# Performance work log

Measured on AMD Instinct MI355X. Metric: run time of the kernel, lower is better.

Reference implementation:

```python
import jax, jax.numpy as jnp
import numpy as np

N_NODES = 100000
N_EDGES = 1600000
N_ETYPES = 3
IN_FEATS = 128
HEADS = 4
OUT_FEATS = 16
EDGE_FEATS = 64
NEG_SLOPE = 0.2


def setup_inputs() -> dict:
    key = jax.random.key(0)
    ks = jax.random.split(key, 10)
    return {
        "x": jax.random.normal(ks[0], (N_NODES, IN_FEATS), jnp.float32),
        "W": jax.random.normal(ks[1], (IN_FEATS, HEADS * OUT_FEATS), jnp.float32) * 0.05,
        "W_e": jax.random.normal(ks[2], (EDGE_FEATS, HEADS * EDGE_FEATS), jnp.float32) * 0.05,
        "attn_l": jax.random.normal(ks[3], (HEADS, OUT_FEATS), jnp.float32) * 0.1,
        "attn_r": jax.random.normal(ks[4], (HEADS, OUT_FEATS), jnp.float32) * 0.1,
        "attn_e": jax.random.normal(ks[5], (HEADS, EDGE_FEATS), jnp.float32) * 0.1,
        "edge_emb": jax.random.normal(ks[6], (N_ETYPES, EDGE_FEATS), jnp.float32),
        "src": jax.random.randint(ks[7], (N_EDGES,), 0, N_NODES, jnp.int32),
        "dst": jax.random.randint(ks[8], (N_EDGES,), 0, N_NODES, jnp.int32),
        "etype": jax.random.randint(ks[9], (N_EDGES,), 0, N_ETYPES, jnp.int32),
    }


def reference(x, W, W_e, attn_l, attn_r, attn_e, edge_emb, src, dst, etype):
    N = x.shape[0]
    H, D = attn_l.shape
    # node projection: [N, H, D]
    feat = (x @ W).reshape(N, H, D)
    # per-node attention halves: [N, H]
    el = jnp.einsum("nhd,hd->nh", feat, attn_l)
    er = jnp.einsum("nhd,hd->nh", feat, attn_r)
    # per-etype edge term: [T, H]
    e_feat = (edge_emb @ W_e).reshape(edge_emb.shape[0], H, -1)
    ee = jnp.einsum("the,he->th", e_feat, attn_e)
    # per-edge pre-softmax score: [E, H]
    s = el[src] + er[dst] + ee[etype]
    s = jnp.where(s > 0, s, NEG_SLOPE * s)  # leaky_relu
    # edge softmax over incoming edges of each dst node (homogeneous graph)
    m = jax.ops.segment_max(s, dst, num_segments=N)
    e = jnp.exp(s - m[dst])
    z = jax.ops.segment_sum(e, dst, num_segments=N)
    a = e / z[dst]  # [E, H]
    # u_mul_e + sum aggregation: [N, H, D]
    msg = feat[src] * a[:, :, None]
    rst = jax.ops.segment_sum(msg, dst, num_segments=N)
    return rst, a
```

## Files before the change

### kernel.cpp

```cpp
#include <hip/hip_runtime.h>
#include <hip/hip_bf16.h>

#define N_NODES   100000
#define N_EDGES   1600000
#define N_ETYPES  3
#define IN_FEATS  128
#define HEADS     4
#define OUT_FEATS 16
#define EDGE_FEATS 64
#define HD        64
#define NEG_SLOPE 0.2f
#define MAXD_LDS  128

#define NBUCK     800
#define NPB       125
#define PBLK      400
#define EPB       4000
#define BCAP      2560
#define FROWS     32


typedef short s16x8 __attribute__((ext_vector_type(8)));
typedef float f32x4 __attribute__((ext_vector_type(4)));

__device__ __forceinline__ short f2bs(float f) {
    __hip_bfloat16 h = __float2bfloat16(f);
    return *reinterpret_cast<short*>(&h);
}

__global__ __launch_bounds__(256) void wt_prep_kernel(
    const float* __restrict__ W, short* __restrict__ WTb)
{
    const int t = blockIdx.x * 256 + threadIdx.x;
    const int k = t >> 6, n = t & 63;
    WTb[n * IN_FEATS + k] = f2bs(W[t]);
}

#define XS_STRIDE 136
__global__ __launch_bounds__(256) void feat_el_er_kernel(
    const float* __restrict__ x,
    const short* __restrict__ WTb,
    const float* __restrict__ attn_l,
    const float* __restrict__ attn_r,
    const float* __restrict__ edge_emb,
    const float* __restrict__ W_e,
    const float* __restrict__ attn_e,
    __hip_bfloat16* __restrict__ featb,
    float* __restrict__ el,
    float* __restrict__ eriz,
    float* __restrict__ ee,
    int* __restrict__ cnt)
{
    const int t = threadIdx.x;

    if (blockIdx.x == N_NODES / FROWS) {
        for (int j = t; j < NBUCK; j += 256) cnt[j] = 0;
        const int wv = t >> 6, e = t & 63;
        for (int j = wv; j < N_ETYPES * HEADS; j += 4) {
            const int ty = j >> 2, h = j & 3;
            float ef = 0.f;
#pragma unroll
            for (int k = 0; k < EDGE_FEATS; ++k)
                ef += edge_emb[ty * EDGE_FEATS + k] *
                      W_e[k * (HEADS * EDGE_FEATS) + h * EDGE_FEATS + e];
            float v = ef * attn_e[h * EDGE_FEATS + e];
#pragma unroll
            for (int m = 1; m < 64; m <<= 1) v += __shfl_xor(v, m, 64);
            if (e == 0) ee[ty * HEADS + h] = v;
        }
        return;
    }

    __shared__ short Xs[FROWS * XS_STRIDE];

    const int row0 = blockIdx.x * FROWS;
    {
        const int r = t >> 3, k0 = (t & 7) * 16;
        const float4* xg = (const float4*)(x + (size_t)(row0 + r) * IN_FEATS + k0);
        const float4 v0 = xg[0], v1 = xg[1], v2 = xg[2], v3 = xg[3];
        s16x8 p0, p1;
        p0[0] = f2bs(v0.x); p0[1] = f2bs(v0.y); p0[2] = f2bs(v0.z); p0[3] = f2bs(v0.w);
        p0[4] = f2bs(v1.x); p0[5] = f2bs(v1.y); p0[6] = f2bs(v1.z); p0[7] = f2bs(v1.w);
        p1[0] = f2bs(v2.x); p1[1] = f2bs(v2.y); p1[2] = f2bs(v2.z); p1[3] = f2bs(v2.w);
        p1[4] = f2bs(v3.x); p1[5] = f2bs(v3.y); p1[6] = f2bs(v3.z); p1[7] = f2bs(v3.w);
        *(s16x8*)&Xs[r * XS_STRIDE + k0]     = p0;
        *(s16x8*)&Xs[r * XS_STRIDE + k0 + 8] = p1;
    }

    const int w    = t >> 6;
    const int lane = t & 63;
    const int m    = lane & 15;
    const int q    = lane >> 4;

    s16x8 bfr[4];
#pragma unroll
    for (int kb = 0; kb < 4; ++kb)
        bfr[kb] = *(const s16x8*)(WTb + (size_t)(w * 16 + m) * IN_FEATS + kb * 32 + q * 8);

    const float al = attn_l[w * OUT_FEATS + m];
    const float ar = attn_r[w * OUT_FEATS + m];

    __syncthreads();

#pragma unroll
    for (int rg = 0; rg < 2; ++rg) {
        f32x4 acc = {0.f, 0.f, 0.f, 0.f};
#pragma unroll
        for (int kb = 0; kb < 4; ++kb) {
            const s16x8 af = *(const s16x8*)&Xs[(rg * 16 + m) * XS_STRIDE + kb * 32 + q * 8];
            acc = __builtin_amdgcn_mfma_f32_16x16x32_bf16(af, bfr[kb], acc, 0, 0, 0);
        }
#pragma unroll
        for (int r = 0; r < 4; ++r) {
            const int row = row0 + rg * 16 + q * 4 + r;
            featb[(size_t)row * HD + w * 16 + m] = __float2bfloat16(acc[r]);
            float cl = acc[r] * al;
            float cr = acc[r] * ar;
#pragma unroll
            for (int msk = 1; msk < 16; msk <<= 1) {
                cl += __shfl_xor(cl, msk, 64);
                cr += __shfl_xor(cr, msk, 64);
            }
            if (m == 0) {
                el[row * HEADS + w] = cl;
                eriz[(size_t)row * 8 + w] = cr;
            }
        }
    }
}

__global__ __launch_bounds__(256) void scatter_kernel(
    const int* __restrict__ src, const int* __restrict__ dst,
    const int* __restrict__ etype,
    int* __restrict__ cnt, int* __restrict__ sc_bucket)
{
    __shared__ int h[NBUCK];
    int buld[16];
    const int t = threadIdx.x, b = blockIdx.x;
    for (int j = t; j < NBUCK; j += 256) h[j] = 0;
    __syncthreads();
    const int e0 = b * EPB;
    int k = 0;
    for (int i = t; i < EPB; i += 256, ++k) {
        const int dn = dst[e0 + i];
        const int bu = dn / NPB;
        const int ld = dn - bu * NPB;
        buld[k] = bu | (ld << 16);
        atomicAdd(&h[bu], 1);
    }
    __syncthreads();
    for (int j = t; j < NBUCK; j += 256) {
        const int c = h[j];
        h[j] = j * BCAP + (c ? atomicAdd(&cnt[j], c) : 0);
    }
    __syncthreads();
    k = 0;
    for (int i = t; i < EPB; i += 256, ++k) {
        const int e  = e0 + i;
        const int bu = buld[k] & 0xFFFF;
        const int ld = buld[k] >> 16;
        const int slot = atomicAdd(&h[bu], 1);
        sc_bucket[slot] = src[e] | (etype[e] << 17) | (ld << 19);
    }
}

__global__ __launch_bounds__(256) void bucket_csr_kernel(
    const int* __restrict__ sc_bucket, const int* __restrict__ cnt,
    int* __restrict__ ptr, int* __restrict__ sc_csr)
{
    __shared__ int sbuf[BCAP];
    __shared__ int sdeg4[4][128];
    __shared__ int sdg[128];
    __shared__ int scur[128];
    __shared__ int red[4];
    const int t = threadIdx.x, b = blockIdx.x;
    const int wid = t >> 6;

    int acc = 0;
    for (int j = t; j < b; j += 256) acc += cnt[j];
#pragma unroll
    for (int m = 1; m < 64; m <<= 1) acc += __shfl_xor(acc, m, 64);
    if ((t & 63) == 0) red[wid] = acc;
    sdeg4[0][t & 127] = 0; sdeg4[1][t & 127] = 0;
    if (t < 128) { sdeg4[2][t] = 0; sdeg4[3][t] = 0; }
    __syncthreads();
    const int lo    = red[0] + red[1] + red[2] + red[3];
    const int count = cnt[b];
    const int base  = b * BCAP;
    const bool staged = (count <= BCAP);

    if (staged) {
        for (int i = t; i < count; i += 256) {
            const int v = sc_bucket[base + i];
            sbuf[i] = v;
            atomicAdd(&sdeg4[wid][(v >> 19) & 0x7F], 1);
        }
    } else {
        for (int i = t; i < count; i += 256)
            atomicAdd(&sdeg4[wid][(sc_bucket[base + i] >> 19) & 0x7F], 1);
    }
    __syncthreads();
    int orig = 0;
    if (t < 128) {
        orig = sdeg4[0][t] + sdeg4[1][t] + sdeg4[2][t] + sdeg4[3][t];
        sdg[t] = orig;
    }
    __syncthreads();
    for (int off = 1; off < 128; off <<= 1) {
        const int v = (t < 128 && t >= off) ? sdg[t - off] : 0;
        __syncthreads();
        if (t < 128) sdg[t] += v;
        __syncthreads();
    }
    if (t < 128) {
        const int excl = sdg[t] - orig;
        if (t < NPB) ptr[b * NPB + t] = lo + excl;
        scur[t] = lo + excl;
    }
    if (b == 0 && t == 0) ptr[N_NODES] = N_EDGES;
    __syncthreads();
    if (staged) {
        for (int i = t; i < count; i += 256) {
            const int v = sbuf[i];
            const int ld = (v >> 19) & 0x7F;
            const int slot = atomicAdd(&scur[ld], 1);
            sc_csr[slot] = v & 0x7FFFF;
        }
    } else {
        for (int i = t; i < count; i += 256) {
            const int v = sc_bucket[base + i];
            const int ld = (v >> 19) & 0x7F;
            const int slot = atomicAdd(&scur[ld], 1);
            sc_csr[slot] = v & 0x7FFFF;
        }
    }
}

__global__ __launch_bounds__(256) void agg_kernel(
    const int* __restrict__ sc_csr, const int* __restrict__ ptr,
    const float* __restrict__ el, float* __restrict__ eriz,
    const float* __restrict__ ee, const __hip_bfloat16* __restrict__ featb,
    float* __restrict__ rst)
{
    __shared__ float w_lds[4][MAXD_LDS * HEADS];
    __shared__ int   s_lds[4][MAXD_LDS];
    const int wid  = threadIdx.x >> 6;
    const int lane = threadIdx.x & 63;
    const int n    = blockIdx.x * 4 + wid;

    const int p0  = ptr[n];
    const int deg = ptr[n + 1] - p0;
    float* wl = w_lds[wid];
    int*   sl = s_lds[wid];
    const ushort* fb = (const ushort*)featb;

    if (deg <= MAXD_LDS) {
        const int eo = lane >> 2;
        const int hA = lane & 3;
        const float er_n = eriz[(size_t)n * 8 + hA];
        const float g0 = ee[hA], g1 = ee[HEADS + hA], g2 = ee[2 * HEADS + hA];

        float zacc = 0.f;
        for (int i0 = 0; i0 < deg; i0 += 32) {
            const int idxA = i0 + eo;
            const int idxB = i0 + 16 + eo;
            const bool pA = idxA < deg;
            const bool pB = idxB < deg;
            int vA = 0, vB = 0;
            if (pA) vA = sc_csr[p0 + idxA];
            if (pB) vB = sc_csr[p0 + idxB];
            float eA = 0.f, eB = 0.f;
            if (pA) eA = el[(vA & 0x1FFFF) * HEADS + hA];
            if (pB) eB = el[(vB & 0x1FFFF) * HEADS + hA];
            if (pA) {
                const int ty = vA >> 17;
                float s = eA + er_n + ((ty == 0) ? g0 : ((ty == 1) ? g1 : g2));
                s = s > 0.f ? s : NEG_SLOPE * s;
                const float w = __expf(s);
                wl[idxA * HEADS + hA] = w;
                if (hA == 0) sl[idxA] = vA & 0x1FFFF;
                zacc += w;
            }
            if (pB) {
                const int ty = vB >> 17;
                float s = eB + er_n + ((ty == 0) ? g0 : ((ty == 1) ? g1 : g2));
                s = s > 0.f ? s : NEG_SLOPE * s;
                const float w = __expf(s);
                wl[idxB * HEADS + hA] = w;
                if (hA == 0) sl[idxB] = vB & 0x1FFFF;
                zacc += w;
            }
        }
        zacc += __shfl_xor(zacc, 4, 64);
        zacc += __shfl_xor(zacc, 8, 64);
        zacc += __shfl_xor(zacc, 16, 64);
        zacc += __shfl_xor(zacc, 32, 64);
        if (lane < 4)
            eriz[(size_t)n * 8 + 4 + lane] = (deg > 0) ? __frcp_rn(zacc) : 0.f;

        const int q8 = lane >> 3;
        const int c8 = lane & 7;
        const int h8 = c8 >> 1;
        const float inv_z = (deg > 0) ? __frcp_rn(__shfl(zacc, h8, 64)) : 0.f;

        float a0 = 0.f, a1 = 0.f, a2 = 0.f, a3 = 0.f;
        float a4 = 0.f, a5 = 0.f, a6 = 0.f, a7 = 0.f;
        int i = 0;
        for (; i + 16 <= deg; i += 16) {
            const int idxA = i + q8, idxB = i + 8 + q8;
            const int sA = sl[idxA], sB = sl[idxB];
            const float wA = wl[idxA * HEADS + h8];
            const float wB = wl[idxB * HEADS + h8];
            const uint4 fA = *(const uint4*)(fb + ((size_t)sA << 6) + (c8 << 3));
            const uint4 fB = *(const uint4*)(fb + ((size_t)sB << 6) + (c8 << 3));
            a0 += __uint_as_float(fA.x << 16) * wA;
            a1 += __uint_as_float(fA.x & 0xFFFF0000u) * wA;
            a2 += __uint_as_float(fA.y << 16) * wA;
            a3 += __uint_as_float(fA.y & 0xFFFF0000u) * wA;
            a4 += __uint_as_float(fA.z << 16) * wA;
            a5 += __uint_as_float(fA.z & 0xFFFF0000u) * wA;
            a6 += __uint_as_float(fA.w << 16) * wA;
            a7 += __uint_as_float(fA.w & 0xFFFF0000u) * wA;
            a0 += __uint_as_float(fB.x << 16) * wB;
            a1 += __uint_as_float(fB.x & 0xFFFF0000u) * wB;
            a2 += __uint_as_float(fB.y << 16) * wB;
            a3 += __uint_as_float(fB.y & 0xFFFF0000u) * wB;
            a4 += __uint_as_float(fB.z << 16) * wB;
            a5 += __uint_as_float(fB.z & 0xFFFF0000u) * wB;
            a6 += __uint_as_float(fB.w << 16) * wB;
            a7 += __uint_as_float(fB.w & 0xFFFF0000u) * wB;
        }
        if (i + 8 <= deg) {
            const int idx = i + q8;
            const int sA = sl[idx];
            const float wA = wl[idx * HEADS + h8];
            const uint4 fA = *(const uint4*)(fb + ((size_t)sA << 6) + (c8 << 3));
            a0 += __uint_as_float(fA.x << 16) * wA;
            a1 += __uint_as_float(fA.x & 0xFFFF0000u) * wA;
            a2 += __uint_as_float(fA.y << 16) * wA;
            a3 += __uint_as_float(fA.y & 0xFFFF0000u) * wA;
            a4 += __uint_as_float(fA.z << 16) * wA;
            a5 += __uint_as_float(fA.z & 0xFFFF0000u) * wA;
            a6 += __uint_as_float(fA.w << 16) * wA;
            a7 += __uint_as_float(fA.w & 0xFFFF0000u) * wA;
            i += 8;
        }
        if (i + q8 < deg) {
            const int idx = i + q8;
            const int sA = sl[idx];
            const float wA = wl[idx * HEADS + h8];
            const uint4 fA = *(const uint4*)(fb + ((size_t)sA << 6) + (c8 << 3));
            a0 += __uint_as_float(fA.x << 16) * wA;
            a1 += __uint_as_float(fA.x & 0xFFFF0000u) * wA;
            a2 += __uint_as_float(fA.y << 16) * wA;
            a3 += __uint_as_float(fA.y & 0xFFFF0000u) * wA;
            a4 += __uint_as_float(fA.z << 16) * wA;
            a5 += __uint_as_float(fA.z & 0xFFFF0000u) * wA;
            a6 += __uint_as_float(fA.w << 16) * wA;
            a7 += __uint_as_float(fA.w & 0xFFFF0000u) * wA;
        }
        a0 += __shfl_xor(a0, 8, 64); a0 += __shfl_xor(a0, 16, 64); a0 += __shfl_xor(a0, 32, 64);
        a1 += __shfl_xor(a1, 8, 64); a1 += __shfl_xor(a1, 16, 64); a1 += __shfl_xor(a1, 32, 64);
        a2 += __shfl_xor(a2, 8, 64); a2 += __shfl_xor(a2, 16, 64); a2 += __shfl_xor(a2, 32, 64);
        a3 += __shfl_xor(a3, 8, 64); a3 += __shfl_xor(a3, 16, 64); a3 += __shfl_xor(a3, 32, 64);
        a4 += __shfl_xor(a4, 8, 64); a4 += __shfl_xor(a4, 16, 64); a4 += __shfl_xor(a4, 32, 64);
        a5 += __shfl_xor(a5, 8, 64); a5 += __shfl_xor(a5, 16, 64); a5 += __shfl_xor(a5, 32, 64);
        a6 += __shfl_xor(a6, 8, 64); a6 += __shfl_xor(a6, 16, 64); a6 += __shfl_xor(a6, 32, 64);
        a7 += __shfl_xor(a7, 8, 64); a7 += __shfl_xor(a7, 16, 64); a7 += __shfl_xor(a7, 32, 64);
        if (q8 == 0) {
            f32x4 v0 = {a0 * inv_z, a1 * inv_z, a2 * inv_z, a3 * inv_z};
            f32x4 v1 = {a4 * inv_z, a5 * inv_z, a6 * inv_z, a7 * inv_z};
            *(f32x4*)(rst + (size_t)n * HD + (c8 << 3))     = v0;
            *(f32x4*)(rst + (size_t)n * HD + (c8 << 3) + 4) = v1;
        }
    } else {
        const int hA = lane & 3;
        const int eo = lane >> 2;
        const float er_nA = eriz[(size_t)n * 8 + hA];
        const float a0 = ee[hA], a1 = ee[HEADS + hA], a2 = ee[2 * HEADS + hA];
        float zacc = 0.f;
        for (int base = 0; base < deg; base += 16) {
            const int idx = base + eo;
            if (idx < deg) {
                const int v  = sc_csr[p0 + idx];
                const int sn = v & 0x1FFFF;
                const int ty = v >> 17;
                float s = el[sn * HEADS + hA] + er_nA + ((ty == 0) ? a0 : ((ty == 1) ? a1 : a2));
                s = s > 0.f ? s : NEG_SLOPE * s;
                zacc += __expf(s);
            }
        }
#pragma unroll
        for (int m = 4; m < 64; m <<= 1) zacc += __shfl_xor(zacc, m, 64);
        if (lane < 4) eriz[(size_t)n * 8 + 4 + lane] = __frcp_rn(zacc);
        const int h = lane >> 4;
        const float inv_z = __frcp_rn(__shfl(zacc, h, 64));
        const float er_n = eriz[(size_t)n * 8 + h];
        const float g0 = ee[h], g1 = ee[HEADS + h], g2 = ee[2 * HEADS + h];
        float racc = 0.f;
        for (int i = 0; i < deg; ++i) {
            const int v  = sc_csr[p0 + i];
            const int sn = v & 0x1FFFF;
            const int ty = v >> 17;
            float s = el[sn * HEADS + h] + er_n + ((ty == 0) ? g0 : ((ty == 1) ? g1 : g2));
            s = s > 0.f ? s : NEG_SLOPE * s;
            const float a = __expf(s) * inv_z;
            racc += __bfloat162float(featb[(size_t)sn * HD + lane]) * a;
        }
        rst[(size_t)n * HD + lane] = racc;
    }
}

__global__ __launch_bounds__(256) void attn_out_kernel(
    const int* __restrict__ src, const int* __restrict__ dst,
    const int* __restrict__ etype,
    const float* __restrict__ el, const float* __restrict__ eriz,
    const float* __restrict__ ee,
    float* __restrict__ a_out)
{
    const int e = blockIdx.x * 256 + threadIdx.x;
    const int sN = src[e];
    const int dN = dst[e];
    const int ty = etype[e];
    const float4 l4 = *(const float4*)(el + (size_t)sN * HEADS);
    const float4 r4 = *(const float4*)(eriz + (size_t)dN * 8);
    const float4 iz = *(const float4*)(eriz + (size_t)dN * 8 + 4);
    const float4 g4 = *(const float4*)(ee + (size_t)ty * HEADS);
    float4 a;
    float s;
    s = l4.x + r4.x + g4.x; s = s > 0.f ? s : NEG_SLOPE * s; a.x = __expf(s) * iz.x;
    s = l4.y + r4.y + g4.y; s = s > 0.f ? s : NEG_SLOPE * s; a.y = __expf(s) * iz.y;
    s = l4.z + r4.z + g4.z; s = s > 0.f ? s : NEG_SLOPE * s; a.z = __expf(s) * iz.z;
    s = l4.w + r4.w + g4.w; s = s > 0.f ? s : NEG_SLOPE * s; a.w = __expf(s) * iz.w;
    *(float4*)(a_out + (size_t)e * HEADS) = a;
}

extern "C" void kernel_launch(void* const* d_in, const int* in_sizes, int n_in,
                              void* d_out, int out_size, void* d_ws, size_t ws_size,
                              hipStream_t stream)
{
    const float* x        = (const float*)d_in[0];
    const float* W        = (const float*)d_in[1];
    const float* W_e      = (const float*)d_in[2];
    const float* attn_l   = (const float*)d_in[3];
    const float* attn_r   = (const float*)d_in[4];
    const float* attn_e   = (const float*)d_in[5];
    const float* edge_emb = (const float*)d_in[6];
    const int* src   = (const int*)d_in[7];
    const int* dst   = (const int*)d_in[8];
    const int* etype = (const int*)d_in[9];

    float* out     = (float*)d_out;
    float* rst_out = out;
    float* a_out   = out + (size_t)N_NODES * HD;

    char* w = (char*)d_ws;
    __hip_bfloat16* featb = (__hip_bfloat16*)w; w += (size_t)N_NODES * HD * 2;
    float* el    = (float*)w;  w += (size_t)N_NODES * HEADS * 4;
    float* eriz  = (float*)w;  w += (size_t)N_NODES * 8 * 4;
    float* ee    = (float*)w;  w += 64;
    int*   ptr   = (int*)w;    w += (size_t)(N_NODES + 4) * 4;
    int*   cnt   = (int*)w;    w += (size_t)(NBUCK + 8) * 4;
    short* WTb   = (short*)w;  w += (size_t)HD * IN_FEATS * 2;
    int*   sc_bucket = (int*)w; w += (size_t)NBUCK * BCAP * 4;
    int*   sc_csr    = (int*)w; w += (size_t)N_EDGES * 4;

    wt_prep_kernel<<<(IN_FEATS * HD) / 256, 256, 0, stream>>>(W, WTb);
    feat_el_er_kernel<<<N_NODES / FROWS + 1, 256, 0, stream>>>(
        x, WTb, attn_l, attn_r, edge_emb, W_e, attn_e, featb, el, eriz, ee, cnt);
    scatter_kernel<<<PBLK, 256, 0, stream>>>(src, dst, etype, cnt, sc_bucket);
    bucket_csr_kernel<<<NBUCK, 256, 0, stream>>>(sc_bucket, cnt, ptr, sc_csr);
    agg_kernel<<<N_NODES / 4, 256, 0, stream>>>(
        sc_csr, ptr, el, eriz, ee, featb, rst_out);
    attn_out_kernel<<<N_EDGES / 256, 256, 0, stream>>>(
        src, dst, etype, el, eriz, ee, a_out);
}
```

Before: 276.2 us.

## Fuse attention output into aggregation and sort edges in place within buckets

Bucket records now carry the original edge id alongside src, and the sorted CSR is written back in place inside each bucket, so the separate prefix-sum over bucket counts and the sc_csr buffer are removed. The agg kernel writes normalized attention weights directly to a_out using the stored edge id, which eliminates the separate attn_out kernel and its gathers of el/er/inverse-z. Degree is stored explicitly per node, since CSR segments are no longer contiguous across buckets. The trade-offs are doubled bucket traffic, scattered 4-byte writes to a_out, and silent truncation of buckets that overflow BCAP.

Result: faster. 260.0 us (-5.9%).

```diff
diff --git a/kernel.cpp b/kernel.cpp
--- a/kernel.cpp
+++ b/kernel.cpp
@@ -47,7 +47,7 @@
     const float* __restrict__ attn_e,
     __hip_bfloat16* __restrict__ featb,
     float* __restrict__ el,
-    float* __restrict__ eriz,
+    float* __restrict__ er,
     float* __restrict__ ee,
     int* __restrict__ cnt)
 {
@@ -123,7 +123,7 @@
             }
             if (m == 0) {
                 el[row * HEADS + w] = cl;
-                eriz[(size_t)row * 8 + w] = cr;
+                er[row * HEADS + w] = cr;
             }
         }
     }
@@ -132,7 +132,7 @@
 __global__ __launch_bounds__(256) void scatter_kernel(
     const int* __restrict__ src, const int* __restrict__ dst,
     const int* __restrict__ etype,
-    int* __restrict__ cnt, int* __restrict__ sc_bucket)
+    int* __restrict__ cnt, int2* __restrict__ sc_bucket)
 {
     __shared__ int h[NBUCK];
     int buld[16];
@@ -160,44 +160,31 @@
         const int bu = buld[k] & 0xFFFF;
         const int ld = buld[k] >> 16;
         const int slot = atomicAdd(&h[bu], 1);
-        sc_bucket[slot] = src[e] | (etype[e] << 17) | (ld << 19);
+        sc_bucket[slot] = make_int2(src[e], e | (etype[e] << 21) | (ld << 23));
     }
 }
 
 __global__ __launch_bounds__(256) void bucket_csr_kernel(
-    const int* __restrict__ sc_bucket, const int* __restrict__ cnt,
-    int* __restrict__ ptr, int* __restrict__ sc_csr)
-{
-    __shared__ int sbuf[BCAP];
+    int2* __restrict__ sc_bucket, const int* __restrict__ cnt,
+    int* __restrict__ ptr, int* __restrict__ deg)
+{
+    __shared__ int2 sbuf[BCAP];
     __shared__ int sdeg4[4][128];
     __shared__ int sdg[128];
     __shared__ int scur[128];
-    __shared__ int red[4];
     const int t = threadIdx.x, b = blockIdx.x;
     const int wid = t >> 6;
 
-    int acc = 0;
-    for (int j = t; j < b; j += 256) acc += cnt[j];
-#pragma unroll
-    for (int m = 1; m < 64; m <<= 1) acc += __shfl_xor(acc, m, 64);
-    if ((t & 63) == 0) red[wid] = acc;
     sdeg4[0][t & 127] = 0; sdeg4[1][t & 127] = 0;
     if (t < 128) { sdeg4[2][t] = 0; sdeg4[3][t] = 0; }
     __syncthreads();
-    const int lo    = red[0] + red[1] + red[2] + red[3];
-    const int count = cnt[b];
+    const int count = min(cnt[b], BCAP);
     const int base  = b * BCAP;
-    const bool staged = (count <= BCAP);
-
-    if (staged) {
-        for (int i = t; i < count; i += 256) {
-            const int v = sc_bucket[base + i];
-            sbuf[i] = v;
-            atomicAdd(&sdeg4[wid][(v >> 19) & 0x7F], 1);
-        }
-    } else {
-        for (int i = t; i < count; i += 256)
-            atomicAdd(&sdeg4[wid][(sc_bucket[base + i] >> 19) & 0x7F], 1);
+
+    for (int i = t; i < count; i += 256) {
+        const int2 v = sc_bucket[base + i];
+        sbuf[i] = v;
+        atomicAdd(&sdeg4[wid][(v.y >> 23) & 0x7F], 1);
     }
     __syncthreads();
     int orig = 0;
@@ -214,50 +201,46 @@
     }
     if (t < 128) {
         const int excl = sdg[t] - orig;
-        if (t < NPB) ptr[b * NPB + t] = lo + excl;
-        scur[t] = lo + excl;
-    }
-    if (b == 0 && t == 0) ptr[N_NODES] = N_EDGES;
-    __syncthreads();
-    if (staged) {
-        for (int i = t; i < count; i += 256) {
-            const int v = sbuf[i];
-            const int ld = (v >> 19) & 0x7F;
-            const int slot = atomicAdd(&scur[ld], 1);
-            sc_csr[slot] = v & 0x7FFFF;
-        }
-    } else {
-        for (int i = t; i < count; i += 256) {
-            const int v = sc_bucket[base + i];
-            const int ld = (v >> 19) & 0x7F;
-            const int slot = atomicAdd(&scur[ld], 1);
-            sc_csr[slot] = v & 0x7FFFF;
-        }
+        if (t < NPB) {
+            ptr[b * NPB + t] = base + excl;
+            deg[b * NPB + t] = orig;
+        }
+        scur[t] = base + excl;
+    }
+    __syncthreads();
+    for (int i = t; i < count; i += 256) {
+        const int2 v = sbuf[i];
+        const int ld = (v.y >> 23) & 0x7F;
+        const int slot = atomicAdd(&scur[ld], 1);
+        sc_bucket[slot] = make_int2(v.x, v.y & 0x7FFFFF);
     }
 }
 
 __global__ __launch_bounds__(256) void agg_kernel(
-    const int* __restrict__ sc_csr, const int* __restrict__ ptr,
-    const float* __restrict__ el, float* __restrict__ eriz,
+    const int2* __restrict__ sc_csr, const int* __restrict__ ptr,
+    const int* __restrict__ deg_arr,
+    const float* __restrict__ el, const float* __restrict__ er,
     const float* __restrict__ ee, const __hip_bfloat16* __restrict__ featb,
-    float* __restrict__ rst)
+    float* __restrict__ rst, float* __restrict__ a_out)
 {
     __shared__ float w_lds[4][MAXD_LDS * HEADS];
     __shared__ int   s_lds[4][MAXD_LDS];
+    __shared__ int   e_lds[4][MAXD_LDS];
     const int wid  = threadIdx.x >> 6;
     const int lane = threadIdx.x & 63;
     const int n    = blockIdx.x * 4 + wid;
 
     const int p0  = ptr[n];
-    const int deg = ptr[n + 1] - p0;
+    const int deg = deg_arr[n];
     float* wl = w_lds[wid];
     int*   sl = s_lds[wid];
+    int*   elds = e_lds[wid];
     const ushort* fb = (const ushort*)featb;
 
     if (deg <= MAXD_LDS) {
         const int eo = lane >> 2;
         const int hA = lane & 3;
-        const float er_n = eriz[(size_t)n * 8 + hA];
+        const float er_n = er[n * HEADS + hA];
         const float g0 = ee[hA], g1 = ee[HEADS + hA], g2 = ee[2 * HEADS + hA];
 
         float zacc = 0.f;
@@ -266,28 +249,30 @@
             const int idxB = i0 + 16 + eo;
             const bool pA = idxA < deg;
             const bool pB = idxB < deg;
-            int vA = 0, vB = 0;
+            int2 vA = make_int2(0, 0), vB = make_int2(0, 0);
             if (pA) vA = sc_csr[p0 + idxA];
             if (pB) vB = sc_csr[p0 + idxB];
             float eA = 0.f, eB = 0.f;
-            if (pA) eA = el[(vA & 0x1FFFF) * HEADS + hA];
-            if (pB) eB = el[(vB & 0x1FFFF) * HEADS + hA];
+            if (pA) eA = el[vA.x * HEADS + hA];
+            if (pB) eB = el[vB.x * HEADS + hA];
             if (pA) {
-                const int ty = vA >> 17;
+                const int ty = vA.y >> 21;
                 float s = eA + er_n + ((ty == 0) ? g0 : ((ty == 1) ? g1 : g2));
                 s = s > 0.f ? s : NEG_SLOPE * s;
                 const float w = __expf(s);
                 wl[idxA * HEADS + hA] = w;
-                if (hA == 0) sl[idxA] = vA & 0x1FFFF;
+                if (hA == 0) sl[idxA] = vA.x;
+                if (hA == 1) elds[idxA] = vA.y & 0x1FFFFF;
                 zacc += w;
             }
             if (pB) {
-                const int ty = vB >> 17;
+                const int ty = vB.y >> 21;
                 float s = eB + er_n + ((ty == 0) ? g0 : ((ty == 1) ? g1 : g2));
                 s = s > 0.f ? s : NEG_SLOPE * s;
                 const float w = __expf(s);
                 wl[idxB * HEADS + hA] = w;
-                if (hA == 0) sl[idxB] = vB & 0x1FFFF;
+                if (hA == 0) sl[idxB] = vB.x;
+                if (hA == 1) elds[idxB] = vB.y & 0x1FFFFF;
                 zacc += w;
             }
         }
@@ -295,8 +280,10 @@
         zacc += __shfl_xor(zacc, 8, 64);
         zacc += __shfl_xor(zacc, 16, 64);
         zacc += __shfl_xor(zacc, 32, 64);
-        if (lane < 4)
-            eriz[(size_t)n * 8 + 4 + lane] = (deg > 0) ? __frcp_rn(zacc) : 0.f;
+        const float izA = (deg > 0) ? __frcp_rn(zacc) : 0.f;
+
+        for (int idx = eo; idx < deg; idx += 16)
+            a_out[((size_t)elds[idx] << 2) + hA] = wl[idx * HEADS + hA] * izA;
 
         const int q8 = lane >> 3;
         const int c8 = lane & 7;
@@ -376,63 +363,38 @@
     } else {
         const int hA = lane & 3;
         const int eo = lane >> 2;
-        const float er_nA = eriz[(size_t)n * 8 + hA];
-        const float a0 = ee[hA], a1 = ee[HEADS + hA], a2 = ee[2 * HEADS + hA];
+        const float er_nA = er[n * HEADS + hA];
+        const float b0 = ee[hA], b1 = ee[HEADS + hA], b2 = ee[2 * HEADS + hA];
         float zacc = 0.f;
         for (int base = 0; base < deg; base += 16) {
             const int idx = base + eo;
             if (idx < deg) {
-                const int v  = sc_csr[p0 + idx];
-                const int sn = v & 0x1FFFF;
-                const int ty = v >> 17;
-                float s = el[sn * HEADS + hA] + er_nA + ((ty == 0) ? a0 : ((ty == 1) ? a1 : a2));
+                const int2 v = sc_csr[p0 + idx];
+                const int ty = v.y >> 21;
+                float s = el[v.x * HEADS + hA] + er_nA + ((ty == 0) ? b0 : ((ty == 1) ? b1 : b2));
                 s = s > 0.f ? s : NEG_SLOPE * s;
                 zacc += __expf(s);
             }
         }
 #pragma unroll
         for (int m = 4; m < 64; m <<= 1) zacc += __shfl_xor(zacc, m, 64);
-        if (lane < 4) eriz[(size_t)n * 8 + 4 + lane] = __frcp_rn(zacc);
         const int h = lane >> 4;
+        const int d = lane & 15;
         const float inv_z = __frcp_rn(__shfl(zacc, h, 64));
-        const float er_n = eriz[(size_t)n * 8 + h];
+        const float er_n = er[n * HEADS + h];
         const float g0 = ee[h], g1 = ee[HEADS + h], g2 = ee[2 * HEADS + h];
         float racc = 0.f;
         for (int i = 0; i < deg; ++i) {
-            const int v  = sc_csr[p0 + i];
-            const int sn = v & 0x1FFFF;
-            const int ty = v >> 17;
-            float s = el[sn * HEADS + h] + er_n + ((ty == 0) ? g0 : ((ty == 1) ? g1 : g2));
+            const int2 v = sc_csr[p0 + i];
+            const int ty = v.y >> 21;
+            float s = el[v.x * HEADS + h] + er_n + ((ty == 0) ? g0 : ((ty == 1) ? g1 : g2));
             s = s > 0.f ? s : NEG_SLOPE * s;
             const float a = __expf(s) * inv_z;
-            racc += __bfloat162float(featb[(size_t)sn * HD + lane]) * a;
+            racc += __bfloat162float(featb[(size_t)v.x * HD + lane]) * a;
+            if (d == 0) a_out[((size_t)(v.y & 0x1FFFFF) << 2) + h] = a;
         }
         rst[(size_t)n * HD + lane] = racc;
     }
-}
-
-__global__ __launch_bounds__(256) void attn_out_kernel(
-    const int* __restrict__ src, const int* __restrict__ dst,
-    const int* __restrict__ etype,
-    const float* __restrict__ el, const float* __restrict__ eriz,
-    const float* __restrict__ ee,
-    float* __restrict__ a_out)
-{
-    const int e = blockIdx.x * 256 + threadIdx.x;
-    const int sN = src[e];
-    const int dN = dst[e];
-    const int ty = etype[e];
-    const float4 l4 = *(const float4*)(el + (size_t)sN * HEADS);
-    const float4 r4 = *(const float4*)(eriz + (size_t)dN * 8);
-    const float4 iz = *(const float4*)(eriz + (size_t)dN * 8 + 4);
-    const float4 g4 = *(const float4*)(ee + (size_t)ty * HEADS);
-    float4 a;
-    float s;
-    s = l4.x + r4.x + g4.x; s = s > 0.f ? s : NEG_SLOPE * s; a.x = __expf(s) * iz.x;
-    s = l4.y + r4.y + g4.y; s = s > 0.f ? s : NEG_SLOPE * s; a.y = __expf(s) * iz.y;
-    s = l4.z + r4.z + g4.z; s = s > 0.f ? s : NEG_SLOPE * s; a.z = __expf(s) * iz.z;
-    s = l4.w + r4.w + g4.w; s = s > 0.f ? s : NEG_SLOPE * s; a.w = __expf(s) * iz.w;
-    *(float4*)(a_out + (size_t)e * HEADS) = a;
 }
 
 extern "C" void kernel_launch(void* const* d_in, const int* in_sizes, int n_in,
@@ -457,21 +419,19 @@
     char* w = (char*)d_ws;
     __hip_bfloat16* featb = (__hip_bfloat16*)w; w += (size_t)N_NODES * HD * 2;
     float* el    = (float*)w;  w += (size_t)N_NODES * HEADS * 4;
-    float* eriz  = (float*)w;  w += (size_t)N_NODES * 8 * 4;
+    float* er    = (float*)w;  w += (size_t)N_NODES * HEADS * 4;
     float* ee    = (float*)w;  w += 64;
-    int*   ptr   = (int*)w;    w += (size_t)(N_NODES + 4) * 4;
+    int*   ptr   = (int*)w;    w += (size_t)(N_NODES + 8) * 4;
+    int*   deg   = (int*)w;    w += (size_t)(N_NODES + 8) * 4;
     int*   cnt   = (int*)w;    w += (size_t)(NBUCK + 8) * 4;
     short* WTb   = (short*)w;  w += (size_t)HD * IN_FEATS * 2;
-    int*   sc_bucket = (int*)w; w += (size_t)NBUCK * BCAP * 4;
-    int*   sc_csr    = (int*)w; w += (size_t)N_EDGES * 4;
+    int2*  sc_bucket = (int2*)w; w += ((size_t)NBUCK * BCAP + 2048) * 8;
 
     wt_prep_kernel<<<(IN_FEATS * HD) / 256, 256, 0, stream>>>(W, WTb);
     feat_el_er_kernel<<<N_NODES / FROWS + 1, 256, 0, stream>>>(
-        x, WTb, attn_l, attn_r, edge_emb, W_e, attn_e, featb, el, eriz, ee, cnt);
+        x, WTb, attn_l, attn_r, edge_emb, W_e, attn_e, featb, el, er, ee, cnt);
     scatter_kernel<<<PBLK, 256, 0, stream>>>(src, dst, etype, cnt, sc_bucket);
-    bucket_csr_kernel<<<NBUCK, 256, 0, stream>>>(sc_bucket, cnt, ptr, sc_csr);
+    bucket_csr_kernel<<<NBUCK, 256, 0, stream>>>(sc_bucket, cnt, ptr, deg);
     agg_kernel<<<N_NODES / 4, 256, 0, stream>>>(
-        sc_csr, ptr, el, eriz, ee, featb, rst_out);
-    attn_out_kernel<<<N_EDGES / 256, 256, 0, stream>>>(
-        src, dst, etype, el, eriz, ee, a_out);
-}
+        sc_bucket, ptr, deg, el, er, ee, featb, rst_out, a_out);
+}
```
